# Optimization experiments

Hardware: AMD Instinct MI355X
Metric: run time of the kernel (lower is better)

Reference implementation:

```python
import jax, jax.numpy as jnp
import numpy as np
from jax import lax

B, SEQ, D, DEPTH = 256, 50, 256, 4
N, K, R = 16, 4, 16  # d_state, d_conv, dt_rank
EPS = 1e-5


def rmsnorm(x, w):
    var = jnp.mean(jnp.square(x), axis=-1, keepdims=True)
    return x * lax.rsqrt(var + EPS) * w


def mamba_mixer(h, in_proj_w, conv_w, conv_b, x_proj_w, dt_proj_w, dt_proj_b, A_log, D_skip, out_proj_w):
    # h: (B, L, D)
    xz = h @ in_proj_w                       # (B, L, 2D)
    x_in, z = jnp.split(xz, 2, axis=-1)      # each (B, L, D)
    # causal depthwise conv1d, kernel K, groups=D
    x_bdl = x_in.transpose(0, 2, 1)          # (B, D, L)
    kern = conv_w[:, None, :]                # (D, 1, K)
    x_c = lax.conv_general_dilated(x_bdl, kern, window_strides=(1,),
                                   padding=[(K - 1, 0)], feature_group_count=D,
                                   dimension_numbers=('NCH', 'OIH', 'NCH'))
    x_c = jax.nn.silu(x_c + conv_b[None, :, None]).transpose(0, 2, 1)  # (B, L, D)
    # input-dependent SSM params
    x_dbl = x_c @ x_proj_w                   # (B, L, R+2N)
    dt = jax.nn.softplus(x_dbl[..., :R] @ dt_proj_w + dt_proj_b)       # (B, L, D)
    Bm = x_dbl[..., R:R + N]                 # (B, L, N)
    Cm = x_dbl[..., R + N:]                  # (B, L, N)
    A = -jnp.exp(A_log)                      # (D, N)
    dA = jnp.exp(dt[..., None] * A)          # (B, L, D, N)
    dBx = (dt * x_c)[..., None] * Bm[:, :, None, :]                    # (B, L, D, N)

    def step(hstate, inp):
        dA_t, dBx_t, C_t = inp
        hstate = dA_t * hstate + dBx_t      # (B, D, N)
        y_t = jnp.einsum('bdn,bn->bd', hstate, C_t)
        return hstate, y_t

    h0 = jnp.zeros((h.shape[0], D, N), dtype=h.dtype)
    xs = (dA.transpose(1, 0, 2, 3), dBx.transpose(1, 0, 2, 3), Cm.transpose(1, 0, 2))
    _, ys = lax.scan(step, h0, xs)           # (L, B, D)
    y = ys.transpose(1, 0, 2) + D_skip * x_c
    y = y * jax.nn.silu(z)
    return y @ out_proj_w                    # (B, L, D)


def setup_inputs() -> dict:
    key = jax.random.key(0)
    ks = jax.random.split(key, 16)
    sc = lambda *s: 0.02
    inp = {
        'x': jax.random.normal(ks[0], (B, SEQ), dtype=jnp.float32),
        'proj_w': jax.random.normal(ks[1], (1, D), dtype=jnp.float32) * 0.5,
        'proj_b': jnp.zeros((D,), dtype=jnp.float32),
        'cls_token': jax.random.normal(ks[2], (1, 1, D), dtype=jnp.float32) * 0.02,
        'pos_embed': jax.random.normal(ks[3], (1, SEQ + 1, D), dtype=jnp.float32) * 0.02,
        'norm_w': jnp.ones((DEPTH, D), dtype=jnp.float32),
        'in_proj_w': jax.random.normal(ks[4], (DEPTH, D, 2 * D), dtype=jnp.float32) * (D ** -0.5),
        'conv_w': jax.random.normal(ks[5], (DEPTH, D, K), dtype=jnp.float32) * 0.3,
        'conv_b': jnp.zeros((DEPTH, D), dtype=jnp.float32),
        'x_proj_w': jax.random.normal(ks[6], (DEPTH, D, R + 2 * N), dtype=jnp.float32) * (D ** -0.5),
        'dt_proj_w': jax.random.normal(ks[7], (DEPTH, R, D), dtype=jnp.float32) * (R ** -0.5),
        'dt_proj_b': jnp.log(jnp.expm1(jnp.full((DEPTH, D), 0.01, dtype=jnp.float32))),
        'A_log': jnp.broadcast_to(jnp.log(jnp.arange(1, N + 1, dtype=jnp.float32)), (DEPTH, D, N)).copy(),
        'D_skip': jnp.ones((DEPTH, D), dtype=jnp.float32),
        'out_proj_w': jax.random.normal(ks[8], (DEPTH, D, D), dtype=jnp.float32) * (D ** -0.5),
        'norm_f_w': jnp.ones((D,), dtype=jnp.float32),
    }
    return inp


def reference(x, proj_w, proj_b, cls_token, pos_embed, norm_w, in_proj_w, conv_w,
              conv_b, x_proj_w, dt_proj_w, dt_proj_b, A_log, D_skip, out_proj_w, norm_f_w):
    # LinearEmbed: (B, SEQ) -> (B, SEQ, 1) -> (B, SEQ, D)
    h = x[..., None] @ proj_w + proj_b
    h = h + pos_embed[:, :-1, :]
    cls = cls_token + pos_embed[:, -1:, :]
    h = jnp.concatenate([jnp.broadcast_to(cls, (h.shape[0], 1, D)), h], axis=1)  # (B, L=51, D)
    residual = None
    for i in range(DEPTH):
        residual = h if residual is None else residual + h
        hn = rmsnorm(residual, norm_w[i])
        h = mamba_mixer(hn, in_proj_w[i], conv_w[i], conv_b[i], x_proj_w[i],
                        dt_proj_w[i], dt_proj_b[i], A_log[i], D_skip[i], out_proj_w[i])
    out = rmsnorm(h, norm_f_w)
    return out[:, 0, :]  # return_type='cls'
```

## Files before the change

kernel.cpp:

```cpp
#include <hip/hip_runtime.h>
#include <math.h>

#define DD 256
#define DEPTH 4
#define WPG 16
#define BPG 17
#define NBLK (DEPTH * BPG)
#define NTHR 256

#define WS_XC   0
#define WS_ZV   256
#define WS_YV   512
#define WS_HV   1024
#define WS_FLAG 2048

#define NX_WX   0
#define NX_WDT  13312
#define NX_DS   17408
#define NX_DB   17664
#define DYN_FLOATS 17920

__device__ __forceinline__ float llc_loadf(const float* p) {
    return __hip_atomic_load(p, __ATOMIC_RELAXED, __HIP_MEMORY_SCOPE_AGENT);
}
__device__ __forceinline__ void llc_storef(float* p, float v) {
    __hip_atomic_store(p, v, __ATOMIC_RELAXED, __HIP_MEMORY_SCOPE_AGENT);
}
__device__ __forceinline__ unsigned llc_loadu(const unsigned* p) {
    return __hip_atomic_load(p, __ATOMIC_RELAXED, __HIP_MEMORY_SCOPE_AGENT);
}
__device__ __forceinline__ void flag_add(unsigned* p) {
    __hip_atomic_fetch_add(p, 1u, __ATOMIC_RELAXED, __HIP_MEMORY_SCOPE_AGENT);
}

__global__ void netmamba_init(unsigned* flags) { flags[threadIdx.x] = 0u; }

__global__ __launch_bounds__(NTHR, 1)
void netmamba_df(const float* __restrict__ cls_token,
                 const float* __restrict__ pos_embed,
                 const float* __restrict__ norm_w,
                 const float* __restrict__ in_proj_w,
                 const float* __restrict__ conv_w,
                 const float* __restrict__ conv_b,
                 const float* __restrict__ x_proj_w,
                 const float* __restrict__ dt_proj_w,
                 const float* __restrict__ dt_proj_b,
                 const float* __restrict__ D_skip,
                 const float* __restrict__ out_proj_w,
                 const float* __restrict__ norm_f_w,
                 float* __restrict__ out,
                 float* __restrict__ ws)
{
    extern __shared__ float dyn[];
    const int tid = threadIdx.x;
    const int bid = blockIdx.x;
    const int g   = bid / BPG;
    const int r   = bid % BPG;
    const bool narrow = (r == WPG);

    float* xc_g = ws + WS_XC;
    float* zv_g = ws + WS_ZV;
    float* yv_g = ws + WS_YV;
    float* hv_g = ws + WS_HV;
    unsigned* flags = (unsigned*)(ws + WS_FLAG);

    __shared__ float sh_a[DD];
    __shared__ float sh_b[DD];
    __shared__ float sh_c[DD];
    __shared__ float sh_d[64];
    __shared__ float red[4];
    __shared__ float rstd_s;

    if (!narrow) {
        const float4* Gi = (const float4*)in_proj_w + (size_t)(g * DD) * 128 + r * 8;
        float4* Li = (float4*)dyn;
        #pragma unroll
        for (int k = 0; k < 8; ++k) {
            const int m = tid + k * 256;
            Li[m] = Gi[(size_t)(m >> 3) * 128 + (m & 7)];
        }
        const float4* Go = (const float4*)out_proj_w + (size_t)(g * DD) * 64 + r * 4;
        float4* Lo = (float4*)(dyn + 8192);
        #pragma unroll
        for (int k = 0; k < 4; ++k) {
            const int m = tid + k * 256;
            Lo[m] = Go[(size_t)(m >> 2) * 64 + (m & 3)];
        }
        if (r < 8 && tid < 32) {
            const int gc = r * 32 + tid;
            sh_d[tid]      = conv_w[((size_t)g * DD + gc) * 4 + 3];
            sh_d[32 + tid] = conv_b[g * DD + gc];
        }
    } else {
        const float4* Gx = (const float4*)x_proj_w + (size_t)(g * DD) * 12;
        #pragma unroll
        for (int k = 0; k < 12; ++k) {
            const int m = tid + k * 256;
            const int d = m / 12, c4 = m % 12;
            *(float4*)(dyn + NX_WX + d * 52 + c4 * 4) = Gx[(size_t)d * 12 + c4];
        }
        const float4* Gd = (const float4*)dt_proj_w + (size_t)g * 1024;
        float4* Ld = (float4*)(dyn + NX_WDT);
        #pragma unroll
        for (int k = 0; k < 4; ++k) { const int m = tid + k * 256; Ld[m] = Gd[m]; }
        dyn[NX_DS + tid] = D_skip[g * DD + tid];
        dyn[NX_DB + tid] = dt_proj_b[g * DD + tid];
    }
    const float nf_reg = norm_f_w[tid];
    float iv_reg = 0.f, nw_reg = 0.f;
    if (!narrow) {
        iv_reg = cls_token[tid] + pos_embed[50 * DD + tid];
        nw_reg = norm_w[g * DD + tid];
    }
    __syncthreads();

    if (!narrow) {
        if (g > 0) {
            if (tid == 0)
                while (llc_loadu(&flags[(8 + g - 1) * 16]) < WPG)
                    __builtin_amdgcn_s_sleep(1);
            __syncthreads();
        }
        float rn = iv_reg;
        for (int l = 0; l < g; ++l) rn += llc_loadf(&hv_g[l * DD + tid]);

        float ss = rn * rn;
        #pragma unroll
        for (int o = 32; o > 0; o >>= 1) ss += __shfl_down(ss, o, 64);
        if ((tid & 63) == 0) red[tid >> 6] = ss;
        __syncthreads();
        if (tid == 0)
            rstd_s = rsqrtf((red[0] + red[1] + red[2] + red[3]) * (1.f / DD) + 1e-5f);
        __syncthreads();
        sh_a[tid] = rn * rstd_s * nw_reg;
        __syncthreads();

        {
            const int c = tid & 31, q = tid >> 5;
            float acc = 0.f;
            #pragma unroll
            for (int i = 0; i < 32; ++i) {
                const int d = q * 32 + i;
                acc += sh_a[d] * dyn[d * 32 + c];
            }
            sh_b[q * 32 + c] = acc;
        }
        __syncthreads();
        if (tid < 32) {
            float s = 0.f;
            #pragma unroll
            for (int p = 0; p < 8; ++p) s += sh_b[p * 32 + tid];
            const int gc = r * 32 + tid;
            if (r < 8) {
                const float pre = sh_d[tid] * s + sh_d[32 + tid];
                llc_storef(&xc_g[gc], pre / (1.f + __expf(-pre)));
            } else {
                llc_storef(&zv_g[gc - DD], s);
            }
        }
        __syncthreads();
        if (tid == 0) flag_add(&flags[g * 16]);

        if (tid == 0)
            while (llc_loadu(&flags[(4 + g) * 16]) < 1)
                __builtin_amdgcn_s_sleep(1);
        __syncthreads();
        sh_c[tid] = llc_loadf(&yv_g[tid]);
        __syncthreads();
        {
            const int c2 = tid & 15, q2 = tid >> 4;
            const float* Lo = dyn + 8192;
            float acc = 0.f;
            #pragma unroll
            for (int i = 0; i < 16; ++i) {
                const int d = i * 16 + q2;
                acc += sh_c[d] * Lo[d * 16 + c2];
            }
            sh_b[q2 * 16 + c2] = acc;
        }
        __syncthreads();
        if (tid < 16) {
            float s = 0.f;
            #pragma unroll
            for (int p = 0; p < 16; ++p) s += sh_b[p * 16 + tid];
            llc_storef(&hv_g[g * DD + r * 16 + tid], s);
        }
        __syncthreads();
        if (tid == 0) flag_add(&flags[(8 + g) * 16]);
    } else {
        if (tid == 0)
            while (llc_loadu(&flags[g * 16]) < WPG)
                __builtin_amdgcn_s_sleep(1);
        __syncthreads();
        sh_a[tid] = llc_loadf(&xc_g[tid]);
        sh_b[tid] = llc_loadf(&zv_g[tid]);
        __syncthreads();
        if (tid < 192) {
            const int j = tid >> 2, q = tid & 3;
            float acc = 0.f;
            #pragma unroll 8
            for (int i = 0; i < 64; ++i) {
                const int d = i * 4 + q;
                acc += sh_a[d] * dyn[NX_WX + d * 52 + j];
            }
            sh_c[j * 4 + q] = acc;
        }
        __syncthreads();
        if (tid < 48)
            sh_d[tid] = sh_c[tid * 4] + sh_c[tid * 4 + 1] + sh_c[tid * 4 + 2] + sh_c[tid * 4 + 3];
        __syncthreads();
        {
            const float* Wdt = dyn + NX_WDT;
            float acc = dyn[NX_DB + tid];
            #pragma unroll
            for (int rr = 0; rr < 16; ++rr) acc += sh_d[rr] * Wdt[rr * 256 + tid];
            const float dtv = fmaxf(acc, 0.f) + log1pf(__expf(-fabsf(acc)));
            float sbc = 0.f;
            #pragma unroll
            for (int n = 0; n < 16; ++n) sbc += sh_d[16 + n] * sh_d[32 + n];
            const float y = (dtv * sbc + dyn[NX_DS + tid]) * sh_a[tid];
            const float z = sh_b[tid];
            llc_storef(&yv_g[tid], y * (z / (1.f + __expf(-z))));
        }
        __syncthreads();
        if (tid == 0) flag_add(&flags[(4 + g) * 16]);
    }

    if (tid == 0)
        while (llc_loadu(&flags[(8 + 3) * 16]) < WPG)
            __builtin_amdgcn_s_sleep(1);
    __syncthreads();
    {
        const float x = llc_loadf(&hv_g[3 * DD + tid]);
        float ss = x * x;
        #pragma unroll
        for (int o = 32; o > 0; o >>= 1) ss += __shfl_down(ss, o, 64);
        if ((tid & 63) == 0) red[tid >> 6] = ss;
        __syncthreads();
        if (tid == 0)
            rstd_s = rsqrtf((red[0] + red[1] + red[2] + red[3]) * (1.f / DD) + 1e-5f);
        __syncthreads();
        sh_a[tid] = x * rstd_s * nf_reg;
    }
    __syncthreads();
    if (bid < 64) {
        const int row = bid * 4 + (tid >> 6);
        const int cc  = tid & 63;
        const float4 v = make_float4(sh_a[cc * 4], sh_a[cc * 4 + 1],
                                     sh_a[cc * 4 + 2], sh_a[cc * 4 + 3]);
        ((float4*)out)[(size_t)row * 64 + cc] = v;
    }
}

extern "C" void kernel_launch(void* const* d_in, const int* in_sizes, int n_in,
                              void* d_out, int out_size, void* d_ws, size_t ws_size,
                              hipStream_t stream) {
    float* ws = (float*)d_ws;
    unsigned* flags = (unsigned*)(ws + WS_FLAG);

    netmamba_init<<<dim3(1), dim3(256), 0, stream>>>(flags);
    netmamba_df<<<dim3(NBLK), dim3(NTHR), DYN_FLOATS * sizeof(float), stream>>>(
        (const float*)d_in[3], (const float*)d_in[4], (const float*)d_in[5],
        (const float*)d_in[6], (const float*)d_in[7], (const float*)d_in[8],
        (const float*)d_in[9], (const float*)d_in[10], (const float*)d_in[11],
        (const float*)d_in[13], (const float*)d_in[14], (const float*)d_in[15],
        (float*)d_out, ws);
}
```

Measured before the change: 43.93 us.

## Merge narrow SSM blocks into wide blocks to cut one inter-block handoff per layer

Removes the dedicated narrow block per layer. Each of the 16 wide blocks now redundantly computes the x_proj, dt, SSM and gating step itself, then immediately does its slice of out_proj. This removes one flag wait and global round-trip from every layer's critical path. The residual is now carried forward as a running sum in the workspace instead of summing all previous layer outputs. Out_proj, x_proj and dt weights are prefetched into larger dynamic shared memory while waiting on the previous layer, at the cost of duplicated small compute and more LDS per block.

```diff
diff --git a/kernel.cpp b/kernel.cpp
--- a/kernel.cpp
+++ b/kernel.cpp
@@ -2,128 +2,126 @@
 #include <math.h>
 
 #define DD 256
-#define DEPTH 4
-#define WPG 16
-#define BPG 17
-#define NBLK (DEPTH * BPG)
+#define NL 4
+#define WPL 16
+#define NBLK (NL * WPL)
 #define NTHR 256
 
 #define WS_XC   0
 #define WS_ZV   256
-#define WS_YV   512
-#define WS_HV   1024
+#define WS_RES  512
+#define WS_HV3  1536
 #define WS_FLAG 2048
 
-#define NX_WX   0
-#define NX_WDT  13312
-#define NX_DS   17408
-#define NX_DB   17664
-#define DYN_FLOATS 17920
-
-__device__ __forceinline__ float llc_loadf(const float* p) {
+#define L_IN  0
+#define L_OUT 8192
+#define L_XP  12288
+#define L_DT  25600
+#define DYN_FLOATS 29696
+
+static __device__ __forceinline__ float llc_loadf(const float* p) {
     return __hip_atomic_load(p, __ATOMIC_RELAXED, __HIP_MEMORY_SCOPE_AGENT);
 }
-__device__ __forceinline__ void llc_storef(float* p, float v) {
+static __device__ __forceinline__ void llc_storef(float* p, float v) {
     __hip_atomic_store(p, v, __ATOMIC_RELAXED, __HIP_MEMORY_SCOPE_AGENT);
 }
-__device__ __forceinline__ unsigned llc_loadu(const unsigned* p) {
+static __device__ __forceinline__ unsigned llc_loadu(const unsigned* p) {
     return __hip_atomic_load(p, __ATOMIC_RELAXED, __HIP_MEMORY_SCOPE_AGENT);
 }
-__device__ __forceinline__ void flag_add(unsigned* p) {
+static __device__ __forceinline__ void flag_add(unsigned* p) {
     __hip_atomic_fetch_add(p, 1u, __ATOMIC_RELAXED, __HIP_MEMORY_SCOPE_AGENT);
 }
 
 __global__ void netmamba_init(unsigned* flags) { flags[threadIdx.x] = 0u; }
 
 __global__ __launch_bounds__(NTHR, 1)
-void netmamba_df(const float* __restrict__ cls_token,
-                 const float* __restrict__ pos_embed,
-                 const float* __restrict__ norm_w,
-                 const float* __restrict__ in_proj_w,
-                 const float* __restrict__ conv_w,
-                 const float* __restrict__ conv_b,
-                 const float* __restrict__ x_proj_w,
-                 const float* __restrict__ dt_proj_w,
-                 const float* __restrict__ dt_proj_b,
-                 const float* __restrict__ D_skip,
-                 const float* __restrict__ out_proj_w,
-                 const float* __restrict__ norm_f_w,
-                 float* __restrict__ out,
-                 float* __restrict__ ws)
+void netmamba_df2(const float* __restrict__ cls_token,
+                  const float* __restrict__ pos_embed,
+                  const float* __restrict__ norm_w,
+                  const float* __restrict__ in_proj_w,
+                  const float* __restrict__ conv_w,
+                  const float* __restrict__ conv_b,
+                  const float* __restrict__ x_proj_w,
+                  const float* __restrict__ dt_proj_w,
+                  const float* __restrict__ dt_proj_b,
+                  const float* __restrict__ D_skip,
+                  const float* __restrict__ out_proj_w,
+                  const float* __restrict__ norm_f_w,
+                  float* __restrict__ out,
+                  float* __restrict__ ws)
 {
     extern __shared__ float dyn[];
     const int tid = threadIdx.x;
     const int bid = blockIdx.x;
-    const int g   = bid / BPG;
-    const int r   = bid % BPG;
-    const bool narrow = (r == WPG);
-
-    float* xc_g = ws + WS_XC;
-    float* zv_g = ws + WS_ZV;
-    float* yv_g = ws + WS_YV;
-    float* hv_g = ws + WS_HV;
+    const int g = bid >> 4;
+    const int r = bid & 15;
+
+    float* xc_g  = ws + WS_XC;
+    float* zv_g  = ws + WS_ZV;
+    float* res_g = ws + WS_RES;
+    float* hv3_g = ws + WS_HV3;
     unsigned* flags = (unsigned*)(ws + WS_FLAG);
 
-    __shared__ float sh_a[DD];
-    __shared__ float sh_b[DD];
-    __shared__ float sh_c[DD];
-    __shared__ float sh_d[64];
+    __shared__ float sh_res[DD];
+    __shared__ float sh_vec[DD];
+    __shared__ float sh_zv[DD];
+    __shared__ float sh_yv[DD];
+    __shared__ float sh_p[DD];
+    __shared__ float sh_x48[48];
+    __shared__ float sh_cv[64];
     __shared__ float red[4];
     __shared__ float rstd_s;
 
-    if (!narrow) {
-        const float4* Gi = (const float4*)in_proj_w + (size_t)(g * DD) * 128 + r * 8;
-        float4* Li = (float4*)dyn;
+    {
+        const float4* Gi = (const float4*)(in_proj_w + (size_t)g * DD * 2 * DD) + r * 8;
         #pragma unroll
         for (int k = 0; k < 8; ++k) {
             const int m = tid + k * 256;
-            Li[m] = Gi[(size_t)(m >> 3) * 128 + (m & 7)];
-        }
-        const float4* Go = (const float4*)out_proj_w + (size_t)(g * DD) * 64 + r * 4;
-        float4* Lo = (float4*)(dyn + 8192);
+            const int d = m >> 3, cg = m & 7;
+            *(float4*)(dyn + L_IN + d * 32 + cg * 4) = Gi[(size_t)d * 128 + cg];
+        }
+        if (r < 8 && tid < 32) {
+            const int gc = g * DD + r * 32 + tid;
+            sh_cv[tid]      = conv_w[(size_t)gc * 4 + 3];
+            sh_cv[32 + tid] = conv_b[gc];
+        }
+    }
+    const float nw  = norm_w[g * DD + tid];
+    const float nf  = norm_f_w[tid];
+    const float dtb = dt_proj_b[g * DD + tid];
+    const float dsk = D_skip[g * DD + tid];
+    const float iv  = cls_token[tid] + pos_embed[50 * DD + tid];
+
+    auto prefetch2 = [&]() {
+        const float4* Go = (const float4*)(out_proj_w + (size_t)g * DD * DD) + r * 4;
         #pragma unroll
         for (int k = 0; k < 4; ++k) {
             const int m = tid + k * 256;
-            Lo[m] = Go[(size_t)(m >> 2) * 64 + (m & 3)];
-        }
-        if (r < 8 && tid < 32) {
-            const int gc = r * 32 + tid;
-            sh_d[tid]      = conv_w[((size_t)g * DD + gc) * 4 + 3];
-            sh_d[32 + tid] = conv_b[g * DD + gc];
-        }
-    } else {
-        const float4* Gx = (const float4*)x_proj_w + (size_t)(g * DD) * 12;
+            const int d = m >> 2, c = m & 3;
+            *(float4*)(dyn + L_OUT + d * 16 + c * 4) = Go[(size_t)d * 64 + c];
+        }
+        const float4* Gx = (const float4*)(x_proj_w + (size_t)g * DD * 48);
         #pragma unroll
         for (int k = 0; k < 12; ++k) {
             const int m = tid + k * 256;
-            const int d = m / 12, c4 = m % 12;
-            *(float4*)(dyn + NX_WX + d * 52 + c4 * 4) = Gx[(size_t)d * 12 + c4];
-        }
-        const float4* Gd = (const float4*)dt_proj_w + (size_t)g * 1024;
-        float4* Ld = (float4*)(dyn + NX_WDT);
+            const int d = m / 12, c4 = m - d * 12;
+            *(float4*)(dyn + L_XP + d * 52 + c4 * 4) = Gx[(size_t)d * 12 + c4];
+        }
+        const float4* Gd = (const float4*)(dt_proj_w + (size_t)g * 16 * DD);
+        float4* Ld = (float4*)(dyn + L_DT);
         #pragma unroll
         for (int k = 0; k < 4; ++k) { const int m = tid + k * 256; Ld[m] = Gd[m]; }
-        dyn[NX_DS + tid] = D_skip[g * DD + tid];
-        dyn[NX_DB + tid] = dt_proj_b[g * DD + tid];
-    }
-    const float nf_reg = norm_f_w[tid];
-    float iv_reg = 0.f, nw_reg = 0.f;
-    if (!narrow) {
-        iv_reg = cls_token[tid] + pos_embed[50 * DD + tid];
-        nw_reg = norm_w[g * DD + tid];
-    }
-    __syncthreads();
-
-    if (!narrow) {
+    };
+
+    auto phaseA = [&]() {
         if (g > 0) {
             if (tid == 0)
-                while (llc_loadu(&flags[(8 + g - 1) * 16]) < WPG)
+                while (llc_loadu(&flags[(4 + g - 1) * 32]) < WPL)
                     __builtin_amdgcn_s_sleep(1);
             __syncthreads();
         }
-        float rn = iv_reg;
-        for (int l = 0; l < g; ++l) rn += llc_loadf(&hv_g[l * DD + tid]);
-
+        const float rn = (g == 0) ? iv : llc_loadf(&res_g[g * DD + tid]);
+        sh_res[tid] = rn;
         float ss = rn * rn;
         #pragma unroll
         for (int o = 32; o > 0; o >>= 1) ss += __shfl_down(ss, o, 64);
@@ -132,7 +130,7 @@
         if (tid == 0)
             rstd_s = rsqrtf((red[0] + red[1] + red[2] + red[3]) * (1.f / DD) + 1e-5f);
         __syncthreads();
-        sh_a[tid] = rn * rstd_s * nw_reg;
+        sh_vec[tid] = rn * rstd_s * nw;
         __syncthreads();
 
         {
@@ -141,97 +139,107 @@
             #pragma unroll
             for (int i = 0; i < 32; ++i) {
                 const int d = q * 32 + i;
-                acc += sh_a[d] * dyn[d * 32 + c];
-            }
-            sh_b[q * 32 + c] = acc;
+                acc += sh_vec[d] * dyn[L_IN + d * 32 + c];
+            }
+            sh_p[q * 32 + c] = acc;
         }
         __syncthreads();
         if (tid < 32) {
             float s = 0.f;
             #pragma unroll
-            for (int p = 0; p < 8; ++p) s += sh_b[p * 32 + tid];
+            for (int p = 0; p < 8; ++p) s += sh_p[p * 32 + tid];
             const int gc = r * 32 + tid;
             if (r < 8) {
-                const float pre = sh_d[tid] * s + sh_d[32 + tid];
+                const float pre = sh_cv[tid] * s + sh_cv[32 + tid];
                 llc_storef(&xc_g[gc], pre / (1.f + __expf(-pre)));
             } else {
                 llc_storef(&zv_g[gc - DD], s);
             }
         }
         __syncthreads();
-        if (tid == 0) flag_add(&flags[g * 16]);
-
+        if (tid == 0) flag_add(&flags[g * 32]);
+    };
+
+    auto phaseB = [&]() {
         if (tid == 0)
-            while (llc_loadu(&flags[(4 + g) * 16]) < 1)
+            while (llc_loadu(&flags[g * 32]) < WPL)
                 __builtin_amdgcn_s_sleep(1);
         __syncthreads();
-        sh_c[tid] = llc_loadf(&yv_g[tid]);
-        __syncthreads();
-        {
-            const int c2 = tid & 15, q2 = tid >> 4;
-            const float* Lo = dyn + 8192;
-            float acc = 0.f;
-            #pragma unroll
-            for (int i = 0; i < 16; ++i) {
-                const int d = i * 16 + q2;
-                acc += sh_c[d] * Lo[d * 16 + c2];
-            }
-            sh_b[q2 * 16 + c2] = acc;
-        }
-        __syncthreads();
-        if (tid < 16) {
-            float s = 0.f;
-            #pragma unroll
-            for (int p = 0; p < 16; ++p) s += sh_b[p * 16 + tid];
-            llc_storef(&hv_g[g * DD + r * 16 + tid], s);
-        }
-        __syncthreads();
-        if (tid == 0) flag_add(&flags[(8 + g) * 16]);
-    } else {
-        if (tid == 0)
-            while (llc_loadu(&flags[g * 16]) < WPG)
-                __builtin_amdgcn_s_sleep(1);
-        __syncthreads();
-        sh_a[tid] = llc_loadf(&xc_g[tid]);
-        sh_b[tid] = llc_loadf(&zv_g[tid]);
-        __syncthreads();
+        sh_vec[tid] = llc_loadf(&xc_g[tid]);
+        sh_zv[tid]  = llc_loadf(&zv_g[tid]);
+        __syncthreads();
+
         if (tid < 192) {
             const int j = tid >> 2, q = tid & 3;
             float acc = 0.f;
             #pragma unroll 8
             for (int i = 0; i < 64; ++i) {
                 const int d = i * 4 + q;
-                acc += sh_a[d] * dyn[NX_WX + d * 52 + j];
-            }
-            sh_c[j * 4 + q] = acc;
+                acc += sh_vec[d] * dyn[L_XP + d * 52 + j];
+            }
+            sh_p[j * 4 + q] = acc;
         }
         __syncthreads();
         if (tid < 48)
-            sh_d[tid] = sh_c[tid * 4] + sh_c[tid * 4 + 1] + sh_c[tid * 4 + 2] + sh_c[tid * 4 + 3];
+            sh_x48[tid] = sh_p[tid * 4] + sh_p[tid * 4 + 1]
+                        + sh_p[tid * 4 + 2] + sh_p[tid * 4 + 3];
         __syncthreads();
         {
-            const float* Wdt = dyn + NX_WDT;
-            float acc = dyn[NX_DB + tid];
-            #pragma unroll
-            for (int rr = 0; rr < 16; ++rr) acc += sh_d[rr] * Wdt[rr * 256 + tid];
+            float acc = dtb;
+            #pragma unroll
+            for (int rr = 0; rr < 16; ++rr)
+                acc += sh_x48[rr] * dyn[L_DT + rr * 256 + tid];
             const float dtv = fmaxf(acc, 0.f) + log1pf(__expf(-fabsf(acc)));
             float sbc = 0.f;
             #pragma unroll
-            for (int n = 0; n < 16; ++n) sbc += sh_d[16 + n] * sh_d[32 + n];
-            const float y = (dtv * sbc + dyn[NX_DS + tid]) * sh_a[tid];
-            const float z = sh_b[tid];
-            llc_storef(&yv_g[tid], y * (z / (1.f + __expf(-z))));
-        }
-        __syncthreads();
-        if (tid == 0) flag_add(&flags[(4 + g) * 16]);
-    }
+            for (int n = 0; n < 16; ++n) sbc += sh_x48[16 + n] * sh_x48[32 + n];
+            const float y = (dtv * sbc + dsk) * sh_vec[tid];
+            const float z = sh_zv[tid];
+            sh_yv[tid] = y * (z / (1.f + __expf(-z)));
+        }
+        __syncthreads();
+
+        {
+            const int c2 = tid & 15, q2 = tid >> 4;
+            float acc = 0.f;
+            #pragma unroll
+            for (int i = 0; i < 16; ++i) {
+                const int d = i * 16 + q2;
+                acc += sh_yv[d] * dyn[L_OUT + d * 16 + c2];
+            }
+            sh_p[q2 * 16 + c2] = acc;
+        }
+        __syncthreads();
+        if (tid < 16) {
+            float s = 0.f;
+            #pragma unroll
+            for (int p = 0; p < 16; ++p) s += sh_p[p * 16 + tid];
+            const int gc = r * 16 + tid;
+            if (g < 3) llc_storef(&res_g[(g + 1) * DD + gc], sh_res[gc] + s);
+            else       llc_storef(&hv3_g[gc], s);
+        }
+        __syncthreads();
+        if (tid == 0) flag_add(&flags[(4 + g) * 32]);
+    };
+
+    if (g == 0) {
+        __syncthreads();
+        phaseA();
+        prefetch2();
+        __syncthreads();
+    } else {
+        prefetch2();
+        __syncthreads();
+        phaseA();
+    }
+    phaseB();
 
     if (tid == 0)
-        while (llc_loadu(&flags[(8 + 3) * 16]) < WPG)
+        while (llc_loadu(&flags[(4 + 3) * 32]) < WPL)
             __builtin_amdgcn_s_sleep(1);
     __syncthreads();
     {
-        const float x = llc_loadf(&hv_g[3 * DD + tid]);
+        const float x = llc_loadf(&hv3_g[tid]);
         float ss = x * x;
         #pragma unroll
         for (int o = 32; o > 0; o >>= 1) ss += __shfl_down(ss, o, 64);
@@ -240,14 +248,14 @@
         if (tid == 0)
             rstd_s = rsqrtf((red[0] + red[1] + red[2] + red[3]) * (1.f / DD) + 1e-5f);
         __syncthreads();
-        sh_a[tid] = x * rstd_s * nf_reg;
+        sh_vec[tid] = x * rstd_s * nf;
     }
     __syncthreads();
-    if (bid < 64) {
+    {
         const int row = bid * 4 + (tid >> 6);
         const int cc  = tid & 63;
-        const float4 v = make_float4(sh_a[cc * 4], sh_a[cc * 4 + 1],
-                                     sh_a[cc * 4 + 2], sh_a[cc * 4 + 3]);
+        const float4 v = make_float4(sh_vec[cc * 4], sh_vec[cc * 4 + 1],
+                                     sh_vec[cc * 4 + 2], sh_vec[cc * 4 + 3]);
         ((float4*)out)[(size_t)row * 64 + cc] = v;
     }
 }
@@ -259,7 +267,7 @@
     unsigned* flags = (unsigned*)(ws + WS_FLAG);
 
     netmamba_init<<<dim3(1), dim3(256), 0, stream>>>(flags);
-    netmamba_df<<<dim3(NBLK), dim3(NTHR), DYN_FLOATS * sizeof(float), stream>>>(
+    netmamba_df2<<<dim3(NBLK), dim3(NTHR), DYN_FLOATS * sizeof(float), stream>>>(
         (const float*)d_in[3], (const float*)d_in[4], (const float*)d_in[5],
         (const float*)d_in[6], (const float*)d_in[7], (const float*)d_in[8],
         (const float*)d_in[9], (const float*)d_in[10], (const float*)d_in[11],
```

After: 38.34 us. -12.7%, faster.
